# Optimization experiments

Measured on AMD Instinct MI355X. Metric: run time of the kernel, lower is better.

Reference implementation:

```python
import jax, jax.numpy as jnp
import numpy as np

B_, L_, O_, N_, S_, U_, DEL, HID, K = 16, 128, 128, 256, 64, 32, 64, 512, 4
D_OUT = DEL + N_ * U_ + N_ * S_  # 24640


def setup_inputs() -> dict:
    key = jax.random.key(0)
    ks = jax.random.split(key, 12)
    return {
        "x": jax.random.normal(ks[0], (B_, O_ + L_, S_), jnp.float32),
        "u": jax.random.normal(ks[1], (B_, 2 * L_, U_), jnp.float32),
        "A": jax.random.normal(ks[2], (N_, 1), jnp.float32) / 20.0,
        "W0": jax.random.normal(ks[3], (HID, S_), jnp.float32) * 0.05,
        "b0": jnp.zeros((HID,), jnp.float32),
        "W1": jax.random.normal(ks[4], (N_, HID), jnp.float32) * 0.05,
        "b1": jnp.zeros((N_,), jnp.float32),
        "conv_w": jax.random.normal(ks[5], (N_ + U_, 1, K), jnp.float32) * 0.3,
        "conv_b": jnp.zeros((N_ + U_,), jnp.float32),
        "Wg": jax.random.normal(ks[6], (D_OUT, N_ + U_), jnp.float32) * 0.05,
        "bg": jnp.zeros((D_OUT,), jnp.float32),
        "Wdt": jax.random.normal(ks[7], (N_, DEL), jnp.float32) * 0.05,
        "bdt": jnp.zeros((N_,), jnp.float32),
    }


def reference(x, u, A, W0, b0, W1, b1, conv_w, conv_b, Wg, bg, Wdt, bdt):
    def proj_x(v):  # Linear -> relu -> Linear (project_x)
        return jax.nn.relu(v @ W0.T + b0) @ W1.T + b1

    u = u[:, :, :U_]
    z0 = proj_x(x[:, O_ - 1, :])                       # (B, N)

    # ---- generate_matrices ----
    x_all = proj_x(x[:, :O_ - 1, :])                   # (B, O-1, N)
    u_all = u[:, :O_ - 1, :]                           # (B, O-1, U)
    old = jax.nn.silu(jnp.concatenate([x_all, u_all], axis=2))  # (B, O-1, N+U)
    old = jnp.transpose(old, (0, 2, 1))                # (B, N+U, O-1)
    old = jax.lax.conv_general_dilated(
        old, conv_w, window_strides=(1,), padding=[(K - 1, K - 1)],
        dimension_numbers=("NCH", "OIH", "NCH"), feature_group_count=N_ + U_,
    ) + conv_b[None, :, None]
    old = old[:, :, -L_:]                              # last L timesteps
    old = jax.nn.silu(jnp.transpose(old, (0, 2, 1)))   # (B, L, N+U)
    gen = old @ Wg.T + bg                              # (B, L, delta + N*U + N*S)
    delta, Bm, Cm = jnp.split(gen, [DEL, DEL + N_ * U_], axis=-1)
    delta = jax.nn.softplus(delta @ Wdt.T + bdt)       # (B, L, N)
    Bm = Bm.reshape(B_, L_, N_, U_)
    Cm = Cm.reshape(B_, L_, N_, S_)

    # ---- discretion_matrices ----
    a = A[:, 0]
    a = -jnp.where(a > 0, a, jnp.expm1(a))             # -celu(A), alpha=1
    dA = jnp.exp(delta * a)                            # (B, L, N)
    dB = ((dA - 1.0) * (1.0 / a))[..., None] * Bm      # (B, L, N, U)

    # ---- selective_scan ----
    u0 = u[:, O_ - 1:O_ - 1 + L_, :]                   # (B, L, U)
    xt = x[:, O_:O_ + L_, :]                           # (B, L, S) targets

    def step(z, inp):
        dAi, dBi, ui, Ci, xti = inp
        z = z * dAi + jnp.einsum("bnu,bu->bn", dBi, ui)
        y = jnp.einsum("bns,bn->bs", Ci, z)
        return z, (y, jnp.mean((y - xti) ** 2))

    xs = (
        jnp.swapaxes(dA, 0, 1), jnp.swapaxes(dB, 0, 1),
        jnp.swapaxes(u0, 0, 1), jnp.swapaxes(Cm, 0, 1), jnp.swapaxes(xt, 0, 1),
    )
    _, (ys, ls) = jax.lax.scan(step, z0, xs)
    loss = jnp.sum(ls) / L_
    return loss, jax.lax.stop_gradient(ys)             # ys: (L, B, S), detached as in torch
```

## Files before the change

kernel.cpp:

```cpp
#include <hip/hip_runtime.h>
#include <math.h>

#define B_   16
#define L_   128
#define O_   128
#define N_   256
#define S_   64
#define U_   32
#define DEL_ 64
#define HID_ 512
#define CH_  288
#define M_   2048
#define KD_  288
#define CM_BASE (DEL_ + N_*U_)
#define NSLICE 32

typedef __bf16 bf16_t;
typedef bf16_t bf16x8 __attribute__((ext_vector_type(8)));
typedef float  f32x4  __attribute__((ext_vector_type(4)));

#define AS1(p) ((const __attribute__((address_space(1))) void*)(unsigned long long)(const void*)(p))
#define AS3(p) ((__attribute__((address_space(3))) void*)(unsigned int)(unsigned long long)(const void*)(p))

__device__ __forceinline__ float silu_f(float x){ return x / (1.f + expf(-x)); }
__device__ __forceinline__ float softplus_f(float x){
  return fmaxf(x, 0.f) + log1pf(expf(-fabsf(x)));
}

__device__ __forceinline__ void cvt8(const float* src, bf16_t* dst){
  float4 a = ((const float4*)src)[0];
  float4 b = ((const float4*)src)[1];
  bf16x8 o;
  o[0]=(bf16_t)a.x; o[1]=(bf16_t)a.y; o[2]=(bf16_t)a.z; o[3]=(bf16_t)a.w;
  o[4]=(bf16_t)b.x; o[5]=(bf16_t)b.y; o[6]=(bf16_t)b.z; o[7]=(bf16_t)b.w;
  *(bf16x8*)dst = o;
}

#define CVT_BLOCKS 3465
#define W0_BLOCKS  16
#define W1_BLOCKS  64
#define XB_BLOCKS  64
__global__ void k_prep(const float* __restrict__ Wg, bf16_t* __restrict__ Wgbf,
                       const float* __restrict__ W0, bf16_t* __restrict__ W0bf,
                       const float* __restrict__ W1, bf16_t* __restrict__ W1bf,
                       const float* __restrict__ x,  bf16_t* __restrict__ xbf,
                       float* __restrict__ lossa){
  if (blockIdx.x == 0 && threadIdx.x < 2) lossa[threadIdx.x] = 0.f;
  if (blockIdx.x < CVT_BLOCKS) {
    int i = blockIdx.x*256 + threadIdx.x;
    if (i >= 887040) return;
    cvt8(Wg + (size_t)i*8, Wgbf + (size_t)i*8);
  } else if (blockIdx.x < CVT_BLOCKS + W0_BLOCKS) {
    int i = (blockIdx.x - CVT_BLOCKS)*256 + threadIdx.x;
    if (i >= 4096) return;
    cvt8(W0 + (size_t)i*8, W0bf + (size_t)i*8);
  } else if (blockIdx.x < CVT_BLOCKS + W0_BLOCKS + W1_BLOCKS) {
    int i = (blockIdx.x - CVT_BLOCKS - W0_BLOCKS)*256 + threadIdx.x;
    if (i >= 16384) return;
    cvt8(W1 + (size_t)i*8, W1bf + (size_t)i*8);
  } else {
    int i = (blockIdx.x - CVT_BLOCKS - W0_BLOCKS - W1_BLOCKS)*256 + threadIdx.x;
    if (i >= 16384) return;
    int m = i >> 3, c0 = (i & 7)*8;
    int b = m >> 7, t = m & 127;
    cvt8(x + (size_t)(((b<<8)+t)<<6) + c0, xbf + (size_t)m*64 + c0);
  }
}

#define STAGE64K(GBASE, ROW0G, STRIDE, KK, LDSP)                                     \
  { const bf16_t* gp_ = (GBASE) + (size_t)((ROW0G) + wave*16 + lm)*(STRIDE) + (KK) + lq*8; \
    __builtin_amdgcn_global_load_lds(AS1(gp_), AS3((LDSP) + wave*512), 16, 0, 0); }

#define STAGE32(GBASE, ROW0G, KK, LDSP)                                              \
  { _Pragma("unroll")                                                                \
    for (int l_ = 0; l_ < 2; l_++) {                                                 \
      int g_ = wave*2 + l_;                                                          \
      const bf16_t* gp_ = (GBASE) + (size_t)((ROW0G) + g_*16 + lm)*KD_ + (KK) + lq*8;\
      __builtin_amdgcn_global_load_lds(AS1(gp_), AS3((LDSP) + g_*512), 16, 0, 0);    \
    } }

#define STAGE_FR96(GBASE, ROW0G, KK, LDSP)                                           \
  { _Pragma("unroll")                                                                \
    for (int c_ = 0; c_ < 3; c_++) {                                                 \
      _Pragma("unroll")                                                              \
      for (int q_ = 0; q_ < 2; q_++) {                                               \
        int g_ = wave*2 + q_;                                                        \
        const bf16_t* gp_ = (GBASE) + (size_t)((ROW0G) + g_*16 + lm)*KD_ + (KK) + c_*32 + lq*8;\
        __builtin_amdgcn_global_load_lds(AS1(gp_), AS3((LDSP) + c_*4096 + g_*512), 16, 0, 0);\
      } } }

__global__ __launch_bounds__(256) void k_mlp1m(
    const bf16_t* __restrict__ xbf, const bf16_t* __restrict__ W0bf,
    const float* __restrict__ b0, bf16_t* __restrict__ Hbf){
  __shared__ __align__(16) bf16_t As[2][2048];
  __shared__ __align__(16) bf16_t Bs[2][2048];
  int tid = threadIdx.x;
  int wave = tid >> 6, lane = tid & 63;
  int wm = wave & 1, wn = wave >> 1;
  int nt = blockIdx.x, mt = blockIdx.y;
  int m0 = mt*64, n0 = nt*64;
  int lm = lane & 15, lq = lane >> 4;

  f32x4 acc[2][2];
  #pragma unroll
  for (int i=0;i<2;i++)
    #pragma unroll
    for (int j=0;j<2;j++){ acc[i][j][0]=0.f;acc[i][j][1]=0.f;acc[i][j][2]=0.f;acc[i][j][3]=0.f; }

  STAGE64K(xbf,  m0, 64, 0, As[0]);
  STAGE64K(W0bf, n0, 64, 0, Bs[0]);
  __syncthreads();
  #pragma unroll
  for (int t = 0; t < 2; ++t) {
    int cur = t & 1;
    if (t < 1) {
      STAGE64K(xbf,  m0, 64, 32, As[1]);
      STAGE64K(W0bf, n0, 64, 32, Bs[1]);
    }
    bf16x8 af[2], bff[2];
    #pragma unroll
    for (int i=0;i<2;i++) af[i]  = *(const bf16x8*)&As[cur][(wm*2 + i)*512 + lane*8];
    #pragma unroll
    for (int j=0;j<2;j++) bff[j] = *(const bf16x8*)&Bs[cur][(wn*2 + j)*512 + lane*8];
    #pragma unroll
    for (int i=0;i<2;i++)
      #pragma unroll
      for (int j=0;j<2;j++)
        acc[i][j] = __builtin_amdgcn_mfma_f32_16x16x32_bf16(af[i], bff[j], acc[i][j], 0,0,0);
    __syncthreads();
  }
  #pragma unroll
  for (int i=0;i<2;i++)
    #pragma unroll
    for (int j=0;j<2;j++){
      int col = n0 + wn*32 + j*16 + lm;
      float bb = b0[col];
      #pragma unroll
      for (int r=0;r<4;r++){
        int row = m0 + wm*32 + i*16 + lq*4 + r;
        Hbf[(size_t)row*HID_ + col] = (bf16_t)fmaxf(acc[i][j][r] + bb, 0.f);
      }
    }
}

__global__ __launch_bounds__(256) void k_mlp2m(
    const bf16_t* __restrict__ Hbf, const bf16_t* __restrict__ W1bf,
    const float* __restrict__ b1, float* __restrict__ P){
  __shared__ __align__(16) bf16_t As[2][2048];
  __shared__ __align__(16) bf16_t Bs[2][2048];
  int tid = threadIdx.x;
  int wave = tid >> 6, lane = tid & 63;
  int wm = wave & 1, wn = wave >> 1;
  int nt = blockIdx.x, mt = blockIdx.y;
  int m0 = mt*64, n0 = nt*64;
  int lm = lane & 15, lq = lane >> 4;

  f32x4 acc[2][2];
  #pragma unroll
  for (int i=0;i<2;i++)
    #pragma unroll
    for (int j=0;j<2;j++){ acc[i][j][0]=0.f;acc[i][j][1]=0.f;acc[i][j][2]=0.f;acc[i][j][3]=0.f; }

  STAGE64K(Hbf,  m0, HID_, 0, As[0]);
  STAGE64K(W1bf, n0, HID_, 0, Bs[0]);
  __syncthreads();
  for (int t = 0; t < 16; ++t) {
    int cur = t & 1;
    if (t < 15) {
      int kk = (t+1)*32;
      STAGE64K(Hbf,  m0, HID_, kk, As[cur^1]);
      STAGE64K(W1bf, n0, HID_, kk, Bs[cur^1]);
    }
    bf16x8 af[2], bff[2];
    #pragma unroll
    for (int i=0;i<2;i++) af[i]  = *(const bf16x8*)&As[cur][(wm*2 + i)*512 + lane*8];
    #pragma unroll
    for (int j=0;j<2;j++) bff[j] = *(const bf16x8*)&Bs[cur][(wn*2 + j)*512 + lane*8];
    #pragma unroll
    for (int i=0;i<2;i++)
      #pragma unroll
      for (int j=0;j<2;j++)
        acc[i][j] = __builtin_amdgcn_mfma_f32_16x16x32_bf16(af[i], bff[j], acc[i][j], 0,0,0);
    __syncthreads();
  }
  #pragma unroll
  for (int i=0;i<2;i++)
    #pragma unroll
    for (int j=0;j<2;j++){
      int col = n0 + wn*32 + j*16 + lm;
      float bb = b1[col];
      #pragma unroll
      for (int r=0;r<4;r++){
        int row = m0 + wm*32 + i*16 + lq*4 + r;
        P[(size_t)row*N_ + col] = acc[i][j][r] + bb;
      }
    }
}

__global__ __launch_bounds__(256) void k_convdelta(
    const float* __restrict__ P, const float* __restrict__ u,
    const float* __restrict__ cw, const float* __restrict__ cb,
    const float* __restrict__ Wg, const float* __restrict__ bg,
    const float* __restrict__ Wdt, const float* __restrict__ bdt,
    const float* __restrict__ Ap, bf16_t* __restrict__ oldbf,
    float* __restrict__ dA, float* __restrict__ coef){
  __shared__ __align__(16) float olds[4*KD_];
  __shared__ float dr[4][64];
  int tid = threadIdx.x;
  int m0 = blockIdx.x * 4;
  int b = m0 >> 7, l0 = m0 & 127;
  for (int e = tid; e < 4*CH_; e += 256) {
    int r = e / CH_, c = e - r*CH_;
    int l = l0 + r;
    float acc = cb[c];
    #pragma unroll
    for (int k = 0; k < 4; k++) {
      int t = l + k - 1;
      if (t >= 0 && t <= O_-2) {
        float s = (c < N_) ? P[((b<<7)+t)*N_ + c] : u[((b<<8)+t)*U_ + (c-N_)];
        acc += silu_f(s) * cw[c*4 + k];
      }
    }
    float v = silu_f(acc);
    olds[e] = v;
    oldbf[(size_t)(m0+r)*CH_ + c] = (bf16_t)v;
  }
  __syncthreads();
  {
    int d = tid & 63;
    int r = tid >> 6;
    const float* wrow = Wg + (size_t)d*KD_;
    const float* orow = olds + r*KD_;
    float s = 0.f;
    for (int k = 0; k < KD_; k++) s += orow[k] * wrow[k];
    dr[r][d] = s + bg[d];
  }
  __syncthreads();
  int n = tid;
  float wrow[64];
  #pragma unroll
  for (int d = 0; d < 64; d++) wrow[d] = Wdt[n*64 + d];
  float a0 = Ap[n];
  float a = -(a0 > 0.f ? a0 : expm1f(a0));
  float inva = 1.f / a;
  float bd = bdt[n];
  #pragma unroll
  for (int r = 0; r < 4; r++) {
    float s = bd;
    #pragma unroll
    for (int d = 0; d < 64; d++) s += dr[r][d] * wrow[d];
    float dd = softplus_f(s);
    float e  = expf(dd * a);
    size_t m = m0 + r;
    dA[m*N_ + n]   = e;
    coef[m*N_ + n] = (e - 1.f) * inva;
  }
}

__global__ __launch_bounds__(256, 2) void k_bmfma(
    const bf16_t* __restrict__ oldbf, const bf16_t* __restrict__ Wgbf,
    const float* __restrict__ bg, const float* __restrict__ u,
    const float* __restrict__ coef, const float* __restrict__ dAg,
    const float* __restrict__ Pg, float* __restrict__ zall){
  __shared__ union {
    struct { __align__(16) bf16_t A[2][4096]; __align__(16) bf16_t B[2][4096]; } st;
    struct { float wl[128][4]; float dal[128][4]; } sc;
  } sm;
  int tid = threadIdx.x;
  int wave = tid >> 6, lane = tid & 63;
  int wm = wave & 1, wn = wave >> 1;
  int mt = blockIdx.y, nt = blockIdx.x;
  int m0 = mt*128, ncol0 = nt*128;
  int lm = lane & 15, lq = lane >> 4;

  f32x4 acc[4][4];
  #pragma unroll
  for (int i=0;i<4;i++)
    #pragma unroll
    for (int j=0;j<4;j++){ acc[i][j][0]=0.f;acc[i][j][1]=0.f;acc[i][j][2]=0.f;acc[i][j][3]=0.f; }

  STAGE32(oldbf, m0, 0, sm.st.A[0]);
  STAGE32(Wgbf, DEL_ + ncol0, 0, sm.st.B[0]);
  __syncthreads();
  for (int t = 0; t < 9; ++t) {
    int cur = t & 1;
    if (t < 8) {
      int kk = (t+1)*32;
      STAGE32(oldbf, m0, kk, sm.st.A[cur^1]);
      STAGE32(Wgbf, DEL_ + ncol0, kk, sm.st.B[cur^1]);
    }
    bf16x8 af[4], bff[4];
    #pragma unroll
    for (int i=0;i<4;i++) af[i]  = *(const bf16x8*)&sm.st.A[cur][(wm*4 + i)*512 + lane*8];
    #pragma unroll
    for (int j=0;j<4;j++) bff[j] = *(const bf16x8*)&sm.st.B[cur][(wn*4 + j)*512 + lane*8];
    #pragma unroll
    for (int i=0;i<4;i++)
      #pragma unroll
      for (int j=0;j<4;j++)
        acc[i][j] = __builtin_amdgcn_mfma_f32_16x16x32_bf16(af[i], bff[j], acc[i][j], 0,0,0);
    __syncthreads();
  }

  for (int e = tid; e < 512; e += 256)
    sm.sc.dal[e>>2][e&3] = dAg[(size_t)(m0 + (e>>2))*N_ + nt*4 + (e&3)];

  float bgv[4];
  #pragma unroll
  for (int j=0;j<4;j++) bgv[j] = bg[DEL_ + ncol0 + wn*64 + j*16 + lm];
  float p[2][4][4];
  #pragma unroll
  for (int a=0;a<2;a++)
    #pragma unroll
    for (int i=0;i<4;i++)
      #pragma unroll
      for (int r=0;r<4;r++) p[a][i][r]=0.f;
  #pragma unroll
  for (int i=0;i<4;i++){
    #pragma unroll
    for (int r=0;r<4;r++){
      int m = m0 + wm*64 + i*16 + lq*4 + r;
      int b = m >> 7, l = m & 127;
      const float* urow = u + ((size_t)(b<<8) + 127 + l)*U_;
      #pragma unroll
      for (int j=0;j<4;j++){
        float uu = urow[(j&1)*16 + lm];
        p[j>>1][i][r] += (acc[i][j][r] + bgv[j]) * uu;
      }
    }
  }
  #pragma unroll
  for (int mk = 1; mk < 16; mk <<= 1){
    #pragma unroll
    for (int a=0;a<2;a++)
      #pragma unroll
      for (int i=0;i<4;i++)
        #pragma unroll
        for (int r=0;r<4;r++) p[a][i][r] += __shfl_xor(p[a][i][r], mk);
  }
  if (lm == 0){
    #pragma unroll
    for (int nl=0;nl<2;nl++){
      int n = ((ncol0 + wn*64 + nl*32) >> 5);
      int nc = wn*2 + nl;
      #pragma unroll
      for (int i=0;i<4;i++)
        #pragma unroll
        for (int r=0;r<4;r++){
          int l = wm*64 + i*16 + lq*4 + r;
          sm.sc.wl[l][nc] = coef[(size_t)(m0+l)*N_ + n] * p[nl][i][r];
        }
    }
  }
  __syncthreads();

  {
    int nc = wave;
    int n = nt*4 + nc;
    float z0 = Pg[(size_t)(m0 + 127)*N_ + n];
    int l0 = lane*2;
    float a0 = sm.sc.dal[l0][nc],   w0 = sm.sc.wl[l0][nc];
    float a1 = sm.sc.dal[l0+1][nc], w1 = sm.sc.wl[l0+1][nc];
    float A = a0*a1, Bv = w0*a1 + w1;
    #pragma unroll
    for (int d = 1; d < 64; d <<= 1){
      float Ap = __shfl_up(A, d);
      float Bp = __shfl_up(Bv, d);
      if (lane >= d){ Bv = Bp*A + Bv; A = Ap*A; }
    }
    float Ae = __shfl_up(A, 1);
    float Be = __shfl_up(Bv, 1);
    if (lane == 0){ Ae = 1.f; Be = 0.f; }
    float zp = z0*Ae + Be;
    float za = zp*a0 + w0;
    float zb = za*a1 + w1;
    zall[(size_t)(m0 + l0)*N_ + n]     = za;
    zall[(size_t)(m0 + l0 + 1)*N_ + n] = zb;
  }
}

__global__ __launch_bounds__(256, 2) void k_cmfma(
    const bf16_t* __restrict__ oldbf, const bf16_t* __restrict__ Wgbf,
    const float* __restrict__ bg, const float* __restrict__ zall,
    float* __restrict__ ypart){
  __shared__ union {
    struct { __align__(16) bf16_t A[3*4096];
             __align__(16) bf16_t Bb[2][3*4096];
             float zl[128][8]; } st;
    float ylds[128][64];
  } sm;
  int tid = threadIdx.x;
  int wave = tid >> 6, lane = tid & 63;
  int wm = wave & 1, wn = wave >> 1;
  int mt = blockIdx.y, grp = blockIdx.x;
  int m0 = mt*128;
  int lm = lane & 15, lq = lane >> 4;

  for (int e = tid; e < 1024; e += 256)
    sm.st.zl[e>>3][e&7] = zall[(size_t)(m0 + (e>>3))*N_ + grp*8 + (e&7)];

  f32x4 yacc[4][4];
  #pragma unroll
  for (int i=0;i<4;i++)
    #pragma unroll
    for (int j=0;j<4;j++){ yacc[i][j][0]=0.f;yacc[i][j][1]=0.f;yacc[i][j][2]=0.f;yacc[i][j][3]=0.f; }

  STAGE_FR96(oldbf, m0, 0, sm.st.A);
  STAGE_FR96(Wgbf, CM_BASE + grp*4*128, 0, sm.st.Bb[0]);
  __syncthreads();

  for (int s = 0; s < 12; ++s) {
    int kh = s >> 2, it = s & 3, cur = s & 1;
    if (s < 11 && it != 3) {
      STAGE_FR96(Wgbf, CM_BASE + (grp*4 + it + 1)*128, kh*96, sm.st.Bb[cur^1]);
    }
    int ncol0 = (grp*4 + it)*128;
    f32x4 acc[4][4];
    #pragma unroll
    for (int i=0;i<4;i++)
      #pragma unroll
      for (int j=0;j<4;j++){ acc[i][j][0]=0.f;acc[i][j][1]=0.f;acc[i][j][2]=0.f;acc[i][j][3]=0.f; }
    for (int c = 0; c < 3; c++) {
      bf16x8 af[4], bff[4];
      #pragma unroll
      for (int i=0;i<4;i++) af[i]  = *(const bf16x8*)&sm.st.A[c*4096 + (wm*4 + i)*512 + lane*8];
      #pragma unroll
      for (int j=0;j<4;j++) bff[j] = *(const bf16x8*)&sm.st.Bb[cur][c*4096 + (wn*4 + j)*512 + lane*8];
      #pragma unroll
      for (int i=0;i<4;i++)
        #pragma unroll
        for (int j=0;j<4;j++)
          acc[i][j] = __builtin_amdgcn_mfma_f32_16x16x32_bf16(af[i], bff[j], acc[i][j], 0,0,0);
    }
    int nl = it*2 + wn;
    float bgv[4];
    #pragma unroll
    for (int j=0;j<4;j++)
      bgv[j] = (kh == 2) ? bg[CM_BASE + ncol0 + wn*64 + j*16 + lm] : 0.f;
    #pragma unroll
    for (int i=0;i<4;i++){
      #pragma unroll
      for (int r=0;r<4;r++){
        float zv = sm.st.zl[wm*64 + i*16 + lq*4 + r][nl];
        #pragma unroll
        for (int j=0;j<4;j++)
          yacc[i][j][r] += (acc[i][j][r] + bgv[j]) * zv;
      }
    }
    __syncthreads();
    if (s < 11 && it == 3) {
      int kk = (kh+1)*96;
      STAGE_FR96(oldbf, m0, kk, sm.st.A);
      STAGE_FR96(Wgbf, CM_BASE + grp*4*128, kk, sm.st.Bb[cur^1]);
      __syncthreads();
    }
  }

  if (wn == 1){
    #pragma unroll
    for (int i=0;i<4;i++)
      #pragma unroll
      for (int j=0;j<4;j++)
        #pragma unroll
        for (int r=0;r<4;r++){
          int ml = wm*64 + i*16 + lq*4 + r;
          sm.ylds[ml][j*16 + lm] = yacc[i][j][r];
        }
  }
  __syncthreads();
  if (wn == 0){
    float* dst = ypart + (size_t)grp*(M_*S_);
    #pragma unroll
    for (int i=0;i<4;i++)
      #pragma unroll
      for (int j=0;j<4;j++)
        #pragma unroll
        for (int r=0;r<4;r++){
          int ml = wm*64 + i*16 + lq*4 + r;
          int s = j*16 + lm;
          dst[(size_t)(m0+ml)*S_ + s] = yacc[i][j][r] + sm.ylds[ml][s];
        }
  }
}

__global__ void k_finalize(const float* __restrict__ ypart, const float* __restrict__ x,
                           float* __restrict__ out, float* __restrict__ lossacc){
  __shared__ float red[256];
  int tid = threadIdx.x;
  float ls = 0.f;
  #pragma unroll
  for (int q = 0; q < 2; q++) {
    int e = blockIdx.x*512 + q*256 + tid;
    int m = e >> 6, s = e & 63;
    int b = m >> 7, l = m & 127;
    float yv = 0.f;
    #pragma unroll 8
    for (int g = 0; g < NSLICE; g++) yv += ypart[(size_t)g*(M_*S_) + e];
    out[1 + (size_t)((l<<4) + b)*S_ + s] = yv;
    float xv = x[((size_t)(b<<8) + 128 + l)*S_ + s];
    float d = yv - xv;
    ls += d*d;
  }
  red[tid] = ls; __syncthreads();
  for (int st = 128; st > 0; st >>= 1) {
    if (tid < st) red[tid] += red[tid+st];
    __syncthreads();
  }
  if (tid == 0) {
    atomicAdd(&lossacc[0], red[0]);
    __threadfence();
    unsigned old = atomicAdd((unsigned*)&lossacc[1], 1u);
    if (old == 255u) {
      float tot = atomicAdd(&lossacc[0], 0.f);
      out[0] = tot * (1.f / (float)(B_*S_*L_));
    }
  }
}

extern "C" void kernel_launch(void* const* d_in, const int* in_sizes, int n_in,
                              void* d_out, int out_size, void* d_ws, size_t ws_size,
                              hipStream_t stream) {
  const float* x   = (const float*)d_in[0];
  const float* u   = (const float*)d_in[1];
  const float* Ap  = (const float*)d_in[2];
  const float* W0  = (const float*)d_in[3];
  const float* b0  = (const float*)d_in[4];
  const float* W1  = (const float*)d_in[5];
  const float* b1  = (const float*)d_in[6];
  const float* cw  = (const float*)d_in[7];
  const float* cb  = (const float*)d_in[8];
  const float* Wg  = (const float*)d_in[9];
  const float* bg  = (const float*)d_in[10];
  const float* Wdt = (const float*)d_in[11];
  const float* bdt = (const float*)d_in[12];
  float* out = (float*)d_out;

  float* ws    = (float*)d_ws;
  float* zall  = ws;
  float* lossa = zall + 524288;
  bf16_t* oldbf = (bf16_t*)(lossa + 512);
  bf16_t* Wgbf  = (bf16_t*)(lossa + 512 + 294912);
  bf16_t* W0bf  = (bf16_t*)(lossa + 512 + 294912 + 3548160);
  bf16_t* W1bf  = (bf16_t*)(lossa + 512 + 294912 + 3548160 + 16384);
  bf16_t* xbf   = (bf16_t*)(lossa + 512 + 294912 + 3548160 + 16384 + 65536);
  bf16_t* Hbf   = (bf16_t*)(lossa + 512 + 294912 + 3548160 + 16384 + 65536 + 65536);
  float* R     = lossa + 512 + 294912 + 3548160 + 16384 + 65536 + 65536 + 524288;
  float* Pp    = R;
  float* dA    = Pp   + 524288;
  float* coef  = dA   + 524288;
  float* ypart = R;

  k_prep<<<CVT_BLOCKS + W0_BLOCKS + W1_BLOCKS + XB_BLOCKS, 256, 0, stream>>>(
      Wg, Wgbf, W0, W0bf, W1, W1bf, x, xbf, lossa);
  k_mlp1m<<<dim3(HID_/64, M_/64), 256, 0, stream>>>(xbf, W0bf, b0, Hbf);
  k_mlp2m<<<dim3(N_/64, M_/64), 256, 0, stream>>>(Hbf, W1bf, b1, Pp);
  k_convdelta<<<M_/4, 256, 0, stream>>>(Pp, u, cw, cb, Wg, bg, Wdt, bdt, Ap,
                                        oldbf, dA, coef);
  k_bmfma<<<dim3(64, 16), 256, 0, stream>>>(oldbf, Wgbf, bg, u, coef, dA, Pp, zall);
  k_cmfma<<<dim3(32, 16), 256, 0, stream>>>(oldbf, Wgbf, bg, zall, ypart);
  k_finalize<<<256, 256, 0, stream>>>(ypart, x, out, lossa);
}
```

Baseline: 206.3 us.

## Retile C-matrix MFMA kernel to 64-row tiles with fine-grained K pipelining

The Cm-projection kernel moves from 128-row tiles with 96-wide K chunks to 64-row tiles staged in 32-wide K slices, double-buffered across a flat loop of 36 steps. The grid doubles and less LDS is used per block, with launch bounds raised to target more occupancy. The convdelta kernel also switches its Wg and Wdt dot-product loads to float4, and k_bmfma's launch bound is raised to 3. The cost is reloading the Wg tiles for twice as many row blocks and a barrier at every step.

```diff
diff --git a/kernel.cpp b/kernel.cpp
--- a/kernel.cpp
+++ b/kernel.cpp
@@ -79,16 +79,6 @@
       __builtin_amdgcn_global_load_lds(AS1(gp_), AS3((LDSP) + g_*512), 16, 0, 0);    \
     } }
 
-#define STAGE_FR96(GBASE, ROW0G, KK, LDSP)                                           \
-  { _Pragma("unroll")                                                                \
-    for (int c_ = 0; c_ < 3; c_++) {                                                 \
-      _Pragma("unroll")                                                              \
-      for (int q_ = 0; q_ < 2; q_++) {                                               \
-        int g_ = wave*2 + q_;                                                        \
-        const bf16_t* gp_ = (GBASE) + (size_t)((ROW0G) + g_*16 + lm)*KD_ + (KK) + c_*32 + lq*8;\
-        __builtin_amdgcn_global_load_lds(AS1(gp_), AS3((LDSP) + c_*4096 + g_*512), 16, 0, 0);\
-      } } }
-
 __global__ __launch_bounds__(256) void k_mlp1m(
     const bf16_t* __restrict__ xbf, const bf16_t* __restrict__ W0bf,
     const float* __restrict__ b0, bf16_t* __restrict__ Hbf){
@@ -229,17 +219,27 @@
   {
     int d = tid & 63;
     int r = tid >> 6;
-    const float* wrow = Wg + (size_t)d*KD_;
-    const float* orow = olds + r*KD_;
+    const float4* wrow4 = (const float4*)(Wg + (size_t)d*KD_);
+    const float4* orow4 = (const float4*)(olds + r*KD_);
     float s = 0.f;
-    for (int k = 0; k < KD_; k++) s += orow[k] * wrow[k];
+    #pragma unroll 9
+    for (int k = 0; k < 72; k++) {
+      float4 w = wrow4[k], o = orow4[k];
+      s += o.x*w.x + o.y*w.y + o.z*w.z + o.w*w.w;
+    }
     dr[r][d] = s + bg[d];
   }
   __syncthreads();
   int n = tid;
   float wrow[64];
-  #pragma unroll
-  for (int d = 0; d < 64; d++) wrow[d] = Wdt[n*64 + d];
+  {
+    const float4* wd4 = (const float4*)(Wdt + (size_t)n*64);
+    #pragma unroll
+    for (int q = 0; q < 16; q++) {
+      float4 w = wd4[q];
+      wrow[q*4+0]=w.x; wrow[q*4+1]=w.y; wrow[q*4+2]=w.z; wrow[q*4+3]=w.w;
+    }
+  }
   float a0 = Ap[n];
   float a = -(a0 > 0.f ? a0 : expm1f(a0));
   float inva = 1.f / a;
@@ -257,7 +257,7 @@
   }
 }
 
-__global__ __launch_bounds__(256, 2) void k_bmfma(
+__global__ __launch_bounds__(256, 3) void k_bmfma(
     const bf16_t* __restrict__ oldbf, const bf16_t* __restrict__ Wgbf,
     const float* __restrict__ bg, const float* __restrict__ u,
     const float* __restrict__ coef, const float* __restrict__ dAg,
@@ -379,91 +379,90 @@
   }
 }
 
-__global__ __launch_bounds__(256, 2) void k_cmfma(
+__global__ __launch_bounds__(256, 4) void k_cmfma(
     const bf16_t* __restrict__ oldbf, const bf16_t* __restrict__ Wgbf,
     const float* __restrict__ bg, const float* __restrict__ zall,
     float* __restrict__ ypart){
   __shared__ union {
-    struct { __align__(16) bf16_t A[3*4096];
-             __align__(16) bf16_t Bb[2][3*4096];
-             float zl[128][8]; } st;
-    float ylds[128][64];
+    struct { __align__(16) bf16_t A[2][2048];
+             __align__(16) bf16_t B[2][4096];
+             float zl[64][8]; } st;
+    float ylds[64][64];
   } sm;
   int tid = threadIdx.x;
   int wave = tid >> 6, lane = tid & 63;
   int wm = wave & 1, wn = wave >> 1;
   int mt = blockIdx.y, grp = blockIdx.x;
-  int m0 = mt*128;
+  int m0 = mt*64;
   int lm = lane & 15, lq = lane >> 4;
 
-  for (int e = tid; e < 1024; e += 256)
+  for (int e = tid; e < 512; e += 256)
     sm.st.zl[e>>3][e&7] = zall[(size_t)(m0 + (e>>3))*N_ + grp*8 + (e&7)];
 
-  f32x4 yacc[4][4];
-  #pragma unroll
-  for (int i=0;i<4;i++)
+  f32x4 yacc[2][4];
+  #pragma unroll
+  for (int i=0;i<2;i++)
     #pragma unroll
     for (int j=0;j<4;j++){ yacc[i][j][0]=0.f;yacc[i][j][1]=0.f;yacc[i][j][2]=0.f;yacc[i][j][3]=0.f; }
 
-  STAGE_FR96(oldbf, m0, 0, sm.st.A);
-  STAGE_FR96(Wgbf, CM_BASE + grp*4*128, 0, sm.st.Bb[0]);
-  __syncthreads();
-
-  for (int s = 0; s < 12; ++s) {
-    int kh = s >> 2, it = s & 3, cur = s & 1;
-    if (s < 11 && it != 3) {
-      STAGE_FR96(Wgbf, CM_BASE + (grp*4 + it + 1)*128, kh*96, sm.st.Bb[cur^1]);
-    }
+  STAGE64K(oldbf, m0, KD_, 0, sm.st.A[0]);
+  STAGE32(Wgbf, CM_BASE + grp*4*128, 0, sm.st.B[0]);
+  __syncthreads();
+
+  for (int it = 0; it < 4; ++it) {
     int ncol0 = (grp*4 + it)*128;
-    f32x4 acc[4][4];
-    #pragma unroll
-    for (int i=0;i<4;i++)
+    f32x4 acc[2][4];
+    #pragma unroll
+    for (int i=0;i<2;i++)
       #pragma unroll
       for (int j=0;j<4;j++){ acc[i][j][0]=0.f;acc[i][j][1]=0.f;acc[i][j][2]=0.f;acc[i][j][3]=0.f; }
-    for (int c = 0; c < 3; c++) {
-      bf16x8 af[4], bff[4];
-      #pragma unroll
-      for (int i=0;i<4;i++) af[i]  = *(const bf16x8*)&sm.st.A[c*4096 + (wm*4 + i)*512 + lane*8];
-      #pragma unroll
-      for (int j=0;j<4;j++) bff[j] = *(const bf16x8*)&sm.st.Bb[cur][c*4096 + (wn*4 + j)*512 + lane*8];
-      #pragma unroll
-      for (int i=0;i<4;i++)
+    for (int t = 0; t < 9; ++t) {
+      int s = it*9 + t, cur = s & 1;
+      if (s < 35) {
+        int t2 = t + 1, it2 = it;
+        if (t2 == 9) { t2 = 0; it2 = it + 1; }
+        int kk2 = t2*32;
+        STAGE64K(oldbf, m0, KD_, kk2, sm.st.A[cur^1]);
+        STAGE32(Wgbf, CM_BASE + (grp*4 + it2)*128, kk2, sm.st.B[cur^1]);
+      }
+      bf16x8 af[2], bff[4];
+      #pragma unroll
+      for (int i=0;i<2;i++) af[i]  = *(const bf16x8*)&sm.st.A[cur][(wm*2 + i)*512 + lane*8];
+      #pragma unroll
+      for (int j=0;j<4;j++) bff[j] = *(const bf16x8*)&sm.st.B[cur][(wn*4 + j)*512 + lane*8];
+      #pragma unroll
+      for (int i=0;i<2;i++)
         #pragma unroll
         for (int j=0;j<4;j++)
           acc[i][j] = __builtin_amdgcn_mfma_f32_16x16x32_bf16(af[i], bff[j], acc[i][j], 0,0,0);
-    }
-    int nl = it*2 + wn;
-    float bgv[4];
-    #pragma unroll
-    for (int j=0;j<4;j++)
-      bgv[j] = (kh == 2) ? bg[CM_BASE + ncol0 + wn*64 + j*16 + lm] : 0.f;
-    #pragma unroll
-    for (int i=0;i<4;i++){
-      #pragma unroll
-      for (int r=0;r<4;r++){
-        float zv = sm.st.zl[wm*64 + i*16 + lq*4 + r][nl];
-        #pragma unroll
-        for (int j=0;j<4;j++)
-          yacc[i][j][r] += (acc[i][j][r] + bgv[j]) * zv;
+      if (t == 8) {
+        int nl = it*2 + wn;
+        float bgv[4];
+        #pragma unroll
+        for (int j=0;j<4;j++) bgv[j] = bg[CM_BASE + ncol0 + wn*64 + j*16 + lm];
+        #pragma unroll
+        for (int i=0;i<2;i++){
+          #pragma unroll
+          for (int r=0;r<4;r++){
+            float zv = sm.st.zl[wm*32 + i*16 + lq*4 + r][nl];
+            #pragma unroll
+            for (int j=0;j<4;j++)
+              yacc[i][j][r] += (acc[i][j][r] + bgv[j]) * zv;
+          }
+        }
       }
-    }
-    __syncthreads();
-    if (s < 11 && it == 3) {
-      int kk = (kh+1)*96;
-      STAGE_FR96(oldbf, m0, kk, sm.st.A);
-      STAGE_FR96(Wgbf, CM_BASE + grp*4*128, kk, sm.st.Bb[cur^1]);
       __syncthreads();
     }
   }
 
   if (wn == 1){
     #pragma unroll
-    for (int i=0;i<4;i++)
+    for (int i=0;i<2;i++)
       #pragma unroll
       for (int j=0;j<4;j++)
         #pragma unroll
         for (int r=0;r<4;r++){
-          int ml = wm*64 + i*16 + lq*4 + r;
+          int ml = wm*32 + i*16 + lq*4 + r;
           sm.ylds[ml][j*16 + lm] = yacc[i][j][r];
         }
   }
@@ -471,12 +470,12 @@
   if (wn == 0){
     float* dst = ypart + (size_t)grp*(M_*S_);
     #pragma unroll
-    for (int i=0;i<4;i++)
+    for (int i=0;i<2;i++)
       #pragma unroll
       for (int j=0;j<4;j++)
         #pragma unroll
         for (int r=0;r<4;r++){
-          int ml = wm*64 + i*16 + lq*4 + r;
+          int ml = wm*32 + i*16 + lq*4 + r;
           int s = j*16 + lm;
           dst[(size_t)(m0+ml)*S_ + s] = yacc[i][j][r] + sm.ylds[ml][s];
         }
@@ -557,6 +556,6 @@
   k_convdelta<<<M_/4, 256, 0, stream>>>(Pp, u, cw, cb, Wg, bg, Wdt, bdt, Ap,
                                         oldbf, dA, coef);
   k_bmfma<<<dim3(64, 16), 256, 0, stream>>>(oldbf, Wgbf, bg, u, coef, dA, Pp, zall);
-  k_cmfma<<<dim3(32, 16), 256, 0, stream>>>(oldbf, Wgbf, bg, zall, ypart);
+  k_cmfma<<<dim3(32, M_/64), 256, 0, stream>>>(oldbf, Wgbf, bg, zall, ypart);
   k_finalize<<<256, 256, 0, stream>>>(ypart, x, out, lossa);
 }
```

Result: slower. 221.2 us (+7.2%).
